# Performance work log

Measured on AMD Instinct MI355X. Metric: run time of the kernel, lower is better.

## Reference

```python
import jax, jax.numpy as jnp
import numpy as np

N_WAY = 5
NKPTS = 17
EMBED = 512
N_SUPPORT = 25  # 5-way 5-shot
N_QUERY = 65536


def setup_inputs() -> dict:
    key = jax.random.key(0)
    ks = jax.random.split(key, 12)
    def lin(k, fan_in, fan_out):
        return jax.random.normal(k, (fan_in, fan_out), jnp.float32) / np.float32(np.sqrt(fan_in))
    return {
        'support_features': jax.random.normal(ks[0], (1, N_SUPPORT, EMBED), jnp.float32),
        'support_keypoints': jax.random.uniform(ks[1], (N_SUPPORT, NKPTS, 2), jnp.float32),
        'query_features': jax.random.normal(ks[2], (N_QUERY, EMBED), jnp.float32),
        'image_coords': jax.random.uniform(ks[3], (N_QUERY, 2), jnp.float32) * 512.0,
        'W1': lin(ks[4], EMBED, EMBED), 'b1': jnp.zeros((EMBED,), jnp.float32),
        'W2': lin(ks[5], EMBED, EMBED), 'b2': jnp.zeros((EMBED,), jnp.float32),
        'Wo1': lin(ks[6], EMBED, EMBED // 2), 'bo1': jnp.zeros((EMBED // 2,), jnp.float32),
        'Wo2': lin(ks[7], EMBED // 2, 2), 'bo2': jnp.zeros((2,), jnp.float32),
        'Wc1': lin(ks[8], EMBED, EMBED // 2), 'bc1': jnp.zeros((EMBED // 2,), jnp.float32),
        'Wc2': lin(ks[9], EMBED // 2, 1), 'bc2': jnp.zeros((1,), jnp.float32),
        'temperature': jnp.float32(1.0),
    }


def reference(support_features, support_keypoints, query_features, image_coords,
              W1, b1, W2, b2, Wo1, bo1, Wo2, bo2, Wc1, bc1, Wc2, bc2, temperature):
    eps = 1e-8
    nkpts = support_keypoints.shape[1]
    n_query = query_features.shape[0]
    D = query_features.shape[-1]

    # --- compute_prototypes (batch_size == 1; per-kpt prototype identical by construction) ---
    sf = support_features.reshape(-1, D)                      # [Ns, D]
    h = jnp.maximum(sf @ W1 + b1, 0.0) @ W2 + b2              # prototype_net MLP
    n_per = h.shape[0] // N_WAY
    proto_way = h.reshape(N_WAY, n_per, D).mean(axis=1)       # [n_way, D]
    prototypes = jnp.broadcast_to(proto_way[:, None, :], (N_WAY, nkpts, D))

    # --- compute_distances: 1 - cosine_sim, scaled by temperature ---
    qn = jnp.linalg.norm(query_features, axis=-1)             # [Nq]
    pn = jnp.linalg.norm(proto_way, axis=-1)                  # [n_way]
    sim = (query_features @ proto_way.T) / jnp.maximum(qn[:, None] * pn[None, :], eps)
    dist_way = (1.0 - sim) / temperature                      # [Nq, n_way]
    distances = jnp.broadcast_to(dist_way[:, :, None], (n_query, N_WAY, nkpts))

    # --- predict_keypoints ---
    # avg over kpts is a no-op (identical per kpt); argmin over ways
    class_predictions = jnp.argmin(dist_way, axis=1)          # [Nq] int
    # softmax over a single scalar == 1.0, so keypoints == offset broadcast over kpts
    offset = jnp.maximum(query_features @ Wo1 + bo1, 0.0) @ Wo2 + bo2   # [Nq, 2]
    conf = jax.nn.sigmoid(jnp.maximum(query_features @ Wc1 + bc1, 0.0) @ Wc2 + bc2)  # [Nq, 1]
    keypoints = jnp.broadcast_to(offset[:, None, :], (n_query, nkpts, 2))
    keypoints = jax.nn.sigmoid(keypoints) * image_coords[:, None, :]    # image_coords provided
    confidence = jnp.broadcast_to(conf, (n_query, nkpts))

    return keypoints, confidence, distances, class_predictions, prototypes
```

## Files before the change

### kernel.cpp

```cpp
#include <hip/hip_runtime.h>
#include <hip/hip_bf16.h>

#define NQ 65536
#define DIM 512
#define HID 256
#define NWAY 5
#define NKPTS 17

typedef short bf16x8 __attribute__((ext_vector_type(8)));
typedef float f32x4 __attribute__((ext_vector_type(4)));
typedef _Float16 half8 __attribute__((ext_vector_type(8)));

static __device__ __forceinline__ unsigned short f2bf(float f) {
    unsigned int x = __float_as_uint(f);
    unsigned int r = (x + 0x7fffu + ((x >> 16) & 1u)) >> 16;
    return (unsigned short)r;
}

static __device__ __forceinline__ void async16(void* l, const void* g) {
    __builtin_amdgcn_global_load_lds(
        (const __attribute__((address_space(1))) unsigned int*)g,
        (__attribute__((address_space(3))) unsigned int*)l, 16, 0, 0);
}

__global__ __launch_bounds__(256) void k_sup(const float* __restrict__ sf,
                                             const float* __restrict__ W1, const float* __restrict__ b1,
                                             float* __restrict__ ws_h1) {
    __shared__ float sfl[512];
    __shared__ float red[4][64];
    int bx = blockIdx.x;
    int s = bx >> 3, cb = bx & 7;
    int t = threadIdx.x;
    if (t < 128) ((float4*)sfl)[t] = ((const float4*)(sf + s * DIM))[t];
    __syncthreads();
    int c = cb * 64 + (t & 63);
    int qd = t >> 6;
    const float* Wp = W1 + (size_t)qd * 128 * DIM + c;
    float acc = 0.0f;
    #pragma unroll 4
    for (int kk = 0; kk < 128; kk++)
        acc += sfl[qd * 128 + kk] * Wp[(size_t)kk * DIM];
    red[qd][t & 63] = acc;
    __syncthreads();
    if (t < 64) {
        float h = red[0][t] + red[1][t] + red[2][t] + red[3][t] + b1[cb * 64 + t];
        ws_h1[s * DIM + cb * 64 + t] = fmaxf(h, 0.0f);
    }
}

__global__ __launch_bounds__(256) void k_mid2(const float* __restrict__ ws_h1,
                                              const float* __restrict__ W2, const float* __restrict__ b2,
                                              const float* __restrict__ Wo1, const float* __restrict__ Wc1,
                                              float* __restrict__ ws_proto, unsigned short* __restrict__ wb) {
    int bx = blockIdx.x;
    int t = threadIdx.x;
    if (bx < 40) {
        __shared__ float ml[512];
        __shared__ float red[4][64];
        int w = bx >> 3, cb = bx & 7;
        for (int i = t; i < 512; i += 256) {
            float sum = 0.0f;
            #pragma unroll
            for (int s5 = 0; s5 < 5; s5++) sum += ws_h1[(w * 5 + s5) * DIM + i];
            ml[i] = sum * 0.2f;
        }
        __syncthreads();
        int c = cb * 64 + (t & 63);
        int qd = t >> 6;
        const float* Wp = W2 + (size_t)qd * 128 * DIM + c;
        float acc = 0.0f;
        #pragma unroll 4
        for (int kk = 0; kk < 128; kk++)
            acc += ml[qd * 128 + kk] * Wp[(size_t)kk * DIM];
        red[qd][t & 63] = acc;
        __syncthreads();
        if (t < 64)
            ws_proto[w * DIM + cb * 64 + t] =
                red[0][t] + red[1][t] + red[2][t] + red[3][t] + b2[cb * 64 + t];
    } else {
        __shared__ unsigned short T[64][72];
        int tb = bx - 40;
        const float* src = (tb < 32) ? Wo1 : Wc1;
        int cofs = (tb < 32) ? 0 : 256;
        int tt = tb & 31;
        int kt = tt >> 2;
        int ct = tt & 3;
        int i = t >> 2;
        int qd = t & 3;
        const float* rp = src + (size_t)(kt * 64 + i) * HID + ct * 64 + qd * 16;
        #pragma unroll
        for (int v = 0; v < 4; v++) {
            float4 x = *(const float4*)(rp + v * 4);
            T[qd * 16 + v * 4 + 0][i] = f2bf(x.x);
            T[qd * 16 + v * 4 + 1][i] = f2bf(x.y);
            T[qd * 16 + v * 4 + 2][i] = f2bf(x.z);
            T[qd * 16 + v * 4 + 3][i] = f2bf(x.w);
        }
        __syncthreads();
        int j = t >> 2;
        int part = t & 3;
        uint4 o0 = *(const uint4*)&T[j][part * 16];
        uint4 o1 = *(const uint4*)&T[j][part * 16 + 8];
        unsigned short* dst = wb + (size_t)(cofs + ct * 64 + j) * DIM + kt * 64 + part * 16;
        *(uint4*)dst = o0;
        *(uint4*)(dst + 8) = o1;
    }
}

__global__ __launch_bounds__(256) void k_prep(const float* __restrict__ qf,
                                              const float* __restrict__ ws_proto,
                                              const float* __restrict__ temp_p,
                                              unsigned short* __restrict__ qbf,
                                              float* __restrict__ out_dist, float* __restrict__ out_class,
                                              float* __restrict__ out_proto) {
    __shared__ float dlds[32 * NWAY];
    int bx = blockIdx.x, t = threadIdx.x;
    int wv = t >> 6, lane = t & 63;

    if (bx < NWAY * NKPTS && t < 128) {
        f32x4 v = *(const f32x4*)(ws_proto + (bx / NKPTS) * DIM + t * 4);
        *(f32x4*)(out_proto + (size_t)bx * DIM + t * 4) = v;
    }

    float p[NWAY][8];
    float pn[NWAY];
    {
        float pp[NWAY];
        #pragma unroll
        for (int w = 0; w < NWAY; w++) {
            f32x4 a = *(const f32x4*)(ws_proto + w * DIM + lane * 8);
            f32x4 b = *(const f32x4*)(ws_proto + w * DIM + lane * 8 + 4);
            p[w][0] = a[0]; p[w][1] = a[1]; p[w][2] = a[2]; p[w][3] = a[3];
            p[w][4] = b[0]; p[w][5] = b[1]; p[w][6] = b[2]; p[w][7] = b[3];
            float s = 0.0f;
            #pragma unroll
            for (int j = 0; j < 8; j++) s += p[w][j] * p[w][j];
            pp[w] = s;
        }
        #pragma unroll
        for (int off = 32; off > 0; off >>= 1) {
            #pragma unroll
            for (int w = 0; w < NWAY; w++) pp[w] += __shfl_xor(pp[w], off, 64);
        }
        #pragma unroll
        for (int w = 0; w < NWAY; w++) pn[w] = sqrtf(pp[w]);
    }
    float invt = 1.0f / temp_p[0];

    int qbase = bx * 32 + wv * 8;
    const float* qp = qf + (size_t)qbase * DIM + lane * 8;
    unsigned short* qb = qbf + (size_t)qbase * DIM + lane * 8;

    float dq[8][NWAY + 1];
    #pragma unroll
    for (int qi = 0; qi < 8; qi++) {
        float4 v0 = *(const float4*)(qp + qi * DIM);
        float4 v1 = *(const float4*)(qp + qi * DIM + 4);
        unsigned int r0 = f2bf(v0.x) | ((unsigned int)f2bf(v0.y) << 16);
        unsigned int r1 = f2bf(v0.z) | ((unsigned int)f2bf(v0.w) << 16);
        unsigned int r2 = f2bf(v1.x) | ((unsigned int)f2bf(v1.y) << 16);
        unsigned int r3 = f2bf(v1.z) | ((unsigned int)f2bf(v1.w) << 16);
        *(uint4*)(qb + qi * DIM) = make_uint4(r0, r1, r2, r3);
        float av[8] = {v0.x, v0.y, v0.z, v0.w, v1.x, v1.y, v1.z, v1.w};
        #pragma unroll
        for (int w = 0; w < NWAY; w++) {
            float s = 0.0f;
            #pragma unroll
            for (int j = 0; j < 8; j++) s += av[j] * p[w][j];
            dq[qi][w] = s;
        }
        float s = 0.0f;
        #pragma unroll
        for (int j = 0; j < 8; j++) s += av[j] * av[j];
        dq[qi][NWAY] = s;
    }
    #pragma unroll
    for (int off = 32; off > 0; off >>= 1) {
        #pragma unroll
        for (int qi = 0; qi < 8; qi++) {
            #pragma unroll
            for (int j = 0; j < NWAY + 1; j++)
                dq[qi][j] += __shfl_xor(dq[qi][j], off, 64);
        }
    }
    if (lane < 8) {
        #pragma unroll
        for (int qi = 0; qi < 8; qi++) {
            if (lane == qi) {
                float qn = sqrtf(dq[qi][NWAY]);
                float mv = 1e30f; int ami = 0;
                #pragma unroll
                for (int w = 0; w < NWAY; w++) {
                    float den = fmaxf(qn * pn[w], 1e-8f);
                    float dd = (1.0f - dq[qi][w] / den) * invt;
                    dlds[(wv * 8 + qi) * NWAY + w] = dd;
                    if (dd < mv) { mv = dd; ami = w; }
                }
                out_class[qbase + qi] = (float)ami;
            }
        }
    }
    __syncthreads();
    int Q0 = bx * 32;
    for (int i = t; i < 32 * NWAY * NKPTS; i += 256) {
        int q2 = i / (NWAY * NKPTS);
        int rem = i - q2 * (NWAY * NKPTS);
        out_dist[(size_t)(Q0 + q2) * (NWAY * NKPTS) + rem] = dlds[q2 * NWAY + rem / NKPTS];
    }
}

__global__ __launch_bounds__(512) void k_gemm(const unsigned short* __restrict__ qbf,
                                              const unsigned short* __restrict__ wb,
                                              const float* __restrict__ bo1, const float* __restrict__ Wo2,
                                              const float* __restrict__ bo2,
                                              const float* __restrict__ bc1, const float* __restrict__ Wc2,
                                              const float* __restrict__ bc2,
                                              const float* __restrict__ ic,
                                              float* __restrict__ out_kp, float* __restrict__ out_conf) {
    __shared__ __align__(16) char smem[81920];
    char* Abase = smem;
    char* Bbase = smem + 16384;

    int mb = blockIdx.x;
    int t = threadIdx.x;
    int wv = t >> 6, lane = t & 63;
    int wr = wv >> 2, wc = wv & 3;
    int r = lane & 15, hq = lane >> 4;

    int srow = lane >> 2;
    int sg = (lane & 3) ^ (srow & 3);
    const unsigned short* Ag = qbf + ((size_t)mb * 128 + wv * 16 + srow) * DIM + sg * 8;
    const unsigned short* Bg = wb + ((size_t)wv * 64 + srow) * DIM + sg * 8;

    f32x4 acc[4][8];
    #pragma unroll
    for (int i2 = 0; i2 < 4; i2++)
        #pragma unroll
        for (int j2 = 0; j2 < 8; j2++) { f32x4 z = {0.0f, 0.0f, 0.0f, 0.0f}; acc[i2][j2] = z; }

    async16(Abase + wv * 1024, Ag);
    #pragma unroll
    for (int i = 0; i < 4; i++)
        async16(Bbase + wv * 4096 + i * 1024, Bg + (size_t)i * 16 * DIM);
    __syncthreads();

    for (int it = 0; it < 16; it++) {
        int par = it & 1;
        if (it < 15) {
            int ko = (it + 1) * 32;
            int np = par ^ 1;
            async16(Abase + np * 8192 + wv * 1024, Ag + ko);
            #pragma unroll
            for (int i = 0; i < 4; i++)
                async16(Bbase + np * 32768 + wv * 4096 + i * 1024, Bg + (size_t)i * 16 * DIM + ko);
        }
        const unsigned short* Ap = (const unsigned short*)(Abase + par * 8192);
        const unsigned short* Bp = (const unsigned short*)(Bbase + par * 32768);
        int sl = (hq ^ (r & 3)) * 8;
        bf16x8 af[4], bfr[8];
        #pragma unroll
        for (int mt = 0; mt < 4; mt++) {
            int m = wr * 64 + mt * 16 + r;
            af[mt] = *(const bf16x8*)(Ap + m * 32 + sl);
        }
        #pragma unroll
        for (int nt = 0; nt < 8; nt++) {
            int c = wc * 128 + nt * 16 + r;
            bfr[nt] = *(const bf16x8*)(Bp + c * 32 + sl);
        }
        #pragma unroll
        for (int mt = 0; mt < 4; mt++)
            #pragma unroll
            for (int nt = 0; nt < 8; nt++)
                acc[mt][nt] = __builtin_amdgcn_mfma_f32_16x16x32_bf16(af[mt], bfr[nt], acc[mt][nt], 0, 0, 0);
        __syncthreads();
    }

    _Float16* hl = (_Float16*)smem;
    float* redf = (float*)(smem + 67584);

    if (wc < 2) {
        #pragma unroll
        for (int nt = 0; nt < 8; nt++) {
            int cl = wc * 128 + nt * 16 + r;
            float bv = bo1[cl];
            #pragma unroll
            for (int mt = 0; mt < 4; mt++)
                #pragma unroll
                for (int rg = 0; rg < 4; rg++) {
                    int ml = wr * 64 + mt * 16 + hq * 4 + rg;
                    hl[ml * 264 + cl] = (_Float16)fmaxf(acc[mt][nt][rg] + bv, 0.0f);
                }
        }
    }
    __syncthreads();
    {
        int q = t & 127, qt = t >> 7;
        float ox = 0.0f, oy = 0.0f;
        #pragma unroll 2
        for (int j0 = 0; j0 < 64; j0 += 8) {
            half8 hv = *(const half8*)(hl + q * 264 + qt * 64 + j0);
            #pragma unroll
            for (int j = 0; j < 8; j++) {
                float2 w2 = *(const float2*)(Wo2 + (qt * 64 + j0 + j) * 2);
                float hf = (float)hv[j];
                ox += hf * w2.x;
                oy += hf * w2.y;
            }
        }
        redf[(qt * 128 + q) * 2] = ox;
        redf[(qt * 128 + q) * 2 + 1] = oy;
    }
    __syncthreads();
    if (t < 128) {
        float sx = bo2[0], sy = bo2[1];
        #pragma unroll
        for (int k2 = 0; k2 < 4; k2++) {
            sx += redf[(k2 * 128 + t) * 2];
            sy += redf[(k2 * 128 + t) * 2 + 1];
        }
        size_t Q = (size_t)mb * 128 + t;
        float2 icv = *(const float2*)(ic + Q * 2);
        float gx = icv.x / (1.0f + __expf(-sx));
        float gy = icv.y / (1.0f + __expf(-sy));
        float2 g2 = make_float2(gx, gy);
        float2* dst = (float2*)(out_kp + Q * 34);
        #pragma unroll
        for (int k2 = 0; k2 < 17; k2++) dst[k2] = g2;
    }
    if (wc >= 2) {
        #pragma unroll
        for (int nt = 0; nt < 8; nt++) {
            int cl = (wc - 2) * 128 + nt * 16 + r;
            float bv = bc1[cl];
            #pragma unroll
            for (int mt = 0; mt < 4; mt++)
                #pragma unroll
                for (int rg = 0; rg < 4; rg++) {
                    int ml = wr * 64 + mt * 16 + hq * 4 + rg;
                    hl[ml * 264 + cl] = (_Float16)fmaxf(acc[mt][nt][rg] + bv, 0.0f);
                }
        }
    }
    __syncthreads();
    {
        int q = t & 127, qt = t >> 7;
        float cs = 0.0f;
        #pragma unroll 2
        for (int j0 = 0; j0 < 64; j0 += 8) {
            half8 hv = *(const half8*)(hl + q * 264 + qt * 64 + j0);
            #pragma unroll
            for (int j = 0; j < 8; j++)
                cs += (float)hv[j] * Wc2[qt * 64 + j0 + j];
        }
        redf[qt * 128 + q] = cs;
    }
    __syncthreads();
    if (t < 128) {
        float s = bc2[0] + redf[t] + redf[128 + t] + redf[256 + t] + redf[384 + t];
        float sg2 = 1.0f / (1.0f + __expf(-s));
        size_t Q = (size_t)mb * 128 + t;
        float* dst = out_conf + Q * 17;
        #pragma unroll
        for (int k2 = 0; k2 < 17; k2++) dst[k2] = sg2;
    }
}

extern "C" void kernel_launch(void* const* d_in, const int* in_sizes, int n_in,
                              void* d_out, int out_size, void* d_ws, size_t ws_size,
                              hipStream_t stream) {
    const float* sf = (const float*)d_in[0];
    const float* qf = (const float*)d_in[2];
    const float* ic = (const float*)d_in[3];
    const float* W1 = (const float*)d_in[4];
    const float* b1 = (const float*)d_in[5];
    const float* W2 = (const float*)d_in[6];
    const float* b2 = (const float*)d_in[7];
    const float* Wo1 = (const float*)d_in[8];
    const float* bo1 = (const float*)d_in[9];
    const float* Wo2 = (const float*)d_in[10];
    const float* bo2 = (const float*)d_in[11];
    const float* Wc1 = (const float*)d_in[12];
    const float* bc1 = (const float*)d_in[13];
    const float* Wc2 = (const float*)d_in[14];
    const float* bc2 = (const float*)d_in[15];
    const float* temp = (const float*)d_in[16];

    float* out = (float*)d_out;
    float* out_kp = out;
    float* out_conf = out + 2228224;
    float* out_dist = out + 3342336;
    float* out_class = out + 8912896;
    float* out_proto = out + 8978432;

    char* ws = (char*)d_ws;
    float* ws_h1 = (float*)ws;
    float* ws_proto = (float*)(ws + 51200);
    unsigned short* ws_wb = (unsigned short*)(ws + 65536);
    unsigned short* ws_qbf = (unsigned short*)(ws + 1048576);

    hipLaunchKernelGGL(k_sup, dim3(200), dim3(256), 0, stream, sf, W1, b1, ws_h1);
    hipLaunchKernelGGL(k_mid2, dim3(104), dim3(256), 0, stream, ws_h1, W2, b2, Wo1, Wc1, ws_proto, ws_wb);
    hipLaunchKernelGGL(k_prep, dim3(2048), dim3(256), 0, stream, qf, ws_proto, temp,
                       ws_qbf, out_dist, out_class, out_proto);
    hipLaunchKernelGGL(k_gemm, dim3(512), dim3(512), 0, stream, ws_qbf, ws_wb,
                       bo1, Wo2, bo2, bc1, Wc2, bc2, ic, out_kp, out_conf);
}
```

Before: 341.0 us.

## Fuse query prep (bf16 convert, cosine distances) into the GEMM kernel

Merges the k_prep kernel into the GEMM kernel. Each block now loads fp32 query rows directly, converts them to bf16 into LDS, and accumulates prototype dot products and norms alongside the MFMA loop. This removes the bf16 query round-trip through workspace (a 64 MB write plus read) and one kernel launch. In exchange, the A-tile staging becomes synchronous register loads instead of async LDS loads, LDS use grows (which may limit occupancy), and the distance output writes now sit in the GEMM epilogue.

```diff
diff --git a/kernel.cpp b/kernel.cpp
--- a/kernel.cpp
+++ b/kernel.cpp
@@ -107,119 +107,26 @@
     }
 }
 
-__global__ __launch_bounds__(256) void k_prep(const float* __restrict__ qf,
-                                              const float* __restrict__ ws_proto,
-                                              const float* __restrict__ temp_p,
-                                              unsigned short* __restrict__ qbf,
-                                              float* __restrict__ out_dist, float* __restrict__ out_class,
-                                              float* __restrict__ out_proto) {
-    __shared__ float dlds[32 * NWAY];
-    int bx = blockIdx.x, t = threadIdx.x;
-    int wv = t >> 6, lane = t & 63;
-
-    if (bx < NWAY * NKPTS && t < 128) {
-        f32x4 v = *(const f32x4*)(ws_proto + (bx / NKPTS) * DIM + t * 4);
-        *(f32x4*)(out_proto + (size_t)bx * DIM + t * 4) = v;
-    }
-
-    float p[NWAY][8];
-    float pn[NWAY];
-    {
-        float pp[NWAY];
-        #pragma unroll
-        for (int w = 0; w < NWAY; w++) {
-            f32x4 a = *(const f32x4*)(ws_proto + w * DIM + lane * 8);
-            f32x4 b = *(const f32x4*)(ws_proto + w * DIM + lane * 8 + 4);
-            p[w][0] = a[0]; p[w][1] = a[1]; p[w][2] = a[2]; p[w][3] = a[3];
-            p[w][4] = b[0]; p[w][5] = b[1]; p[w][6] = b[2]; p[w][7] = b[3];
-            float s = 0.0f;
-            #pragma unroll
-            for (int j = 0; j < 8; j++) s += p[w][j] * p[w][j];
-            pp[w] = s;
-        }
-        #pragma unroll
-        for (int off = 32; off > 0; off >>= 1) {
-            #pragma unroll
-            for (int w = 0; w < NWAY; w++) pp[w] += __shfl_xor(pp[w], off, 64);
-        }
-        #pragma unroll
-        for (int w = 0; w < NWAY; w++) pn[w] = sqrtf(pp[w]);
-    }
-    float invt = 1.0f / temp_p[0];
-
-    int qbase = bx * 32 + wv * 8;
-    const float* qp = qf + (size_t)qbase * DIM + lane * 8;
-    unsigned short* qb = qbf + (size_t)qbase * DIM + lane * 8;
-
-    float dq[8][NWAY + 1];
-    #pragma unroll
-    for (int qi = 0; qi < 8; qi++) {
-        float4 v0 = *(const float4*)(qp + qi * DIM);
-        float4 v1 = *(const float4*)(qp + qi * DIM + 4);
-        unsigned int r0 = f2bf(v0.x) | ((unsigned int)f2bf(v0.y) << 16);
-        unsigned int r1 = f2bf(v0.z) | ((unsigned int)f2bf(v0.w) << 16);
-        unsigned int r2 = f2bf(v1.x) | ((unsigned int)f2bf(v1.y) << 16);
-        unsigned int r3 = f2bf(v1.z) | ((unsigned int)f2bf(v1.w) << 16);
-        *(uint4*)(qb + qi * DIM) = make_uint4(r0, r1, r2, r3);
-        float av[8] = {v0.x, v0.y, v0.z, v0.w, v1.x, v1.y, v1.z, v1.w};
-        #pragma unroll
-        for (int w = 0; w < NWAY; w++) {
-            float s = 0.0f;
-            #pragma unroll
-            for (int j = 0; j < 8; j++) s += av[j] * p[w][j];
-            dq[qi][w] = s;
-        }
-        float s = 0.0f;
-        #pragma unroll
-        for (int j = 0; j < 8; j++) s += av[j] * av[j];
-        dq[qi][NWAY] = s;
-    }
-    #pragma unroll
-    for (int off = 32; off > 0; off >>= 1) {
-        #pragma unroll
-        for (int qi = 0; qi < 8; qi++) {
-            #pragma unroll
-            for (int j = 0; j < NWAY + 1; j++)
-                dq[qi][j] += __shfl_xor(dq[qi][j], off, 64);
-        }
-    }
-    if (lane < 8) {
-        #pragma unroll
-        for (int qi = 0; qi < 8; qi++) {
-            if (lane == qi) {
-                float qn = sqrtf(dq[qi][NWAY]);
-                float mv = 1e30f; int ami = 0;
-                #pragma unroll
-                for (int w = 0; w < NWAY; w++) {
-                    float den = fmaxf(qn * pn[w], 1e-8f);
-                    float dd = (1.0f - dq[qi][w] / den) * invt;
-                    dlds[(wv * 8 + qi) * NWAY + w] = dd;
-                    if (dd < mv) { mv = dd; ami = w; }
-                }
-                out_class[qbase + qi] = (float)ami;
-            }
-        }
-    }
-    __syncthreads();
-    int Q0 = bx * 32;
-    for (int i = t; i < 32 * NWAY * NKPTS; i += 256) {
-        int q2 = i / (NWAY * NKPTS);
-        int rem = i - q2 * (NWAY * NKPTS);
-        out_dist[(size_t)(Q0 + q2) * (NWAY * NKPTS) + rem] = dlds[q2 * NWAY + rem / NKPTS];
-    }
-}
-
-__global__ __launch_bounds__(512) void k_gemm(const unsigned short* __restrict__ qbf,
-                                              const unsigned short* __restrict__ wb,
-                                              const float* __restrict__ bo1, const float* __restrict__ Wo2,
-                                              const float* __restrict__ bo2,
-                                              const float* __restrict__ bc1, const float* __restrict__ Wc2,
-                                              const float* __restrict__ bc2,
-                                              const float* __restrict__ ic,
-                                              float* __restrict__ out_kp, float* __restrict__ out_conf) {
-    __shared__ __align__(16) char smem[81920];
+__global__ __launch_bounds__(512, 2) void k_fused2(const float* __restrict__ qf,
+                                                   const unsigned short* __restrict__ wb,
+                                                   const float* __restrict__ ws_proto,
+                                                   const float* __restrict__ temp_p,
+                                                   const float* __restrict__ bo1, const float* __restrict__ Wo2,
+                                                   const float* __restrict__ bo2,
+                                                   const float* __restrict__ bc1, const float* __restrict__ Wc2,
+                                                   const float* __restrict__ bc2,
+                                                   const float* __restrict__ ic,
+                                                   float* __restrict__ out_kp, float* __restrict__ out_conf,
+                                                   float* __restrict__ out_dist, float* __restrict__ out_class,
+                                                   float* __restrict__ out_proto) {
+    __shared__ __align__(16) char smem[94752];
     char* Abase = smem;
     char* Bbase = smem + 16384;
+    float* s_proto = (float*)(smem + 81920);
+    float* pn_lds = (float*)(smem + 92160);
+    float* dlds = (float*)(smem + 92192);
+    _Float16* hl = (_Float16*)smem;
+    float* redf = (float*)(smem + 67584);
 
     int mb = blockIdx.x;
     int t = threadIdx.x;
@@ -227,58 +134,92 @@
     int wr = wv >> 2, wc = wv & 3;
     int r = lane & 15, hq = lane >> 4;
 
+    for (int i = t; i < NWAY * DIM; i += 512) s_proto[i] = ws_proto[i];
+    if (mb < NWAY * NKPTS && t < 128) {
+        f32x4 v = *(const f32x4*)(ws_proto + (mb / NKPTS) * DIM + t * 4);
+        *(f32x4*)(out_proto + (size_t)mb * DIM + t * 4) = v;
+    }
+    float invt = 1.0f / temp_p[0];
+
     int srow = lane >> 2;
     int sg = (lane & 3) ^ (srow & 3);
-    const unsigned short* Ag = qbf + ((size_t)mb * 128 + wv * 16 + srow) * DIM + sg * 8;
     const unsigned short* Bg = wb + ((size_t)wv * 64 + srow) * DIM + sg * 8;
+
+    int am = t >> 2, akc = t & 3;
+    const float* Ag = qf + ((size_t)mb * 128 + am) * DIM + akc * 8;
+    int awoff = am * 64 + ((akc ^ (am & 3)) * 16);
 
     f32x4 acc[4][8];
     #pragma unroll
     for (int i2 = 0; i2 < 4; i2++)
         #pragma unroll
         for (int j2 = 0; j2 < 8; j2++) { f32x4 z = {0.0f, 0.0f, 0.0f, 0.0f}; acc[i2][j2] = z; }
-
-    async16(Abase + wv * 1024, Ag);
+    float ds[NWAY] = {0, 0, 0, 0, 0};
+    float qq = 0.0f;
+
+    float4 a0 = *(const float4*)(Ag);
+    float4 a1 = *(const float4*)(Ag + 4);
     #pragma unroll
     for (int i = 0; i < 4; i++)
         async16(Bbase + wv * 4096 + i * 1024, Bg + (size_t)i * 16 * DIM);
-    __syncthreads();
-
+
+    #pragma unroll 2
     for (int it = 0; it < 16; it++) {
         int par = it & 1;
+        unsigned int p0 = f2bf(a0.x) | ((unsigned int)f2bf(a0.y) << 16);
+        unsigned int p1 = f2bf(a0.z) | ((unsigned int)f2bf(a0.w) << 16);
+        unsigned int p2 = f2bf(a1.x) | ((unsigned int)f2bf(a1.y) << 16);
+        unsigned int p3 = f2bf(a1.z) | ((unsigned int)f2bf(a1.w) << 16);
+        *(uint4*)(Abase + par * 8192 + awoff) = make_uint4(p0, p1, p2, p3);
+        float av[8] = {a0.x, a0.y, a0.z, a0.w, a1.x, a1.y, a1.z, a1.w};
+        int kb = it * 32 + akc * 8;
+        #pragma unroll
+        for (int w = 0; w < NWAY; w++) {
+            f32x4 pv0 = *(const f32x4*)(s_proto + w * DIM + kb);
+            f32x4 pv1 = *(const f32x4*)(s_proto + w * DIM + kb + 4);
+            ds[w] += av[0] * pv0[0] + av[1] * pv0[1] + av[2] * pv0[2] + av[3] * pv0[3]
+                   + av[4] * pv1[0] + av[5] * pv1[1] + av[6] * pv1[2] + av[7] * pv1[3];
+        }
+        #pragma unroll
+        for (int j = 0; j < 8; j++) qq += av[j] * av[j];
         if (it < 15) {
             int ko = (it + 1) * 32;
-            int np = par ^ 1;
-            async16(Abase + np * 8192 + wv * 1024, Ag + ko);
+            a0 = *(const float4*)(Ag + ko);
+            a1 = *(const float4*)(Ag + ko + 4);
             #pragma unroll
             for (int i = 0; i < 4; i++)
-                async16(Bbase + np * 32768 + wv * 4096 + i * 1024, Bg + (size_t)i * 16 * DIM + ko);
-        }
+                async16(Bbase + (par ^ 1) * 32768 + wv * 4096 + i * 1024,
+                        Bg + (size_t)i * 16 * DIM + ko);
+        }
+        __syncthreads();
         const unsigned short* Ap = (const unsigned short*)(Abase + par * 8192);
         const unsigned short* Bp = (const unsigned short*)(Bbase + par * 32768);
         int sl = (hq ^ (r & 3)) * 8;
         bf16x8 af[4], bfr[8];
         #pragma unroll
-        for (int mt = 0; mt < 4; mt++) {
-            int m = wr * 64 + mt * 16 + r;
-            af[mt] = *(const bf16x8*)(Ap + m * 32 + sl);
-        }
-        #pragma unroll
-        for (int nt = 0; nt < 8; nt++) {
-            int c = wc * 128 + nt * 16 + r;
-            bfr[nt] = *(const bf16x8*)(Bp + c * 32 + sl);
-        }
+        for (int mt = 0; mt < 4; mt++)
+            af[mt] = *(const bf16x8*)(Ap + (wr * 64 + mt * 16 + r) * 32 + sl);
+        #pragma unroll
+        for (int nt = 0; nt < 8; nt++)
+            bfr[nt] = *(const bf16x8*)(Bp + (wc * 128 + nt * 16 + r) * 32 + sl);
         #pragma unroll
         for (int mt = 0; mt < 4; mt++)
             #pragma unroll
             for (int nt = 0; nt < 8; nt++)
                 acc[mt][nt] = __builtin_amdgcn_mfma_f32_16x16x32_bf16(af[mt], bfr[nt], acc[mt][nt], 0, 0, 0);
-        __syncthreads();
-    }
-
-    _Float16* hl = (_Float16*)smem;
-    float* redf = (float*)(smem + 67584);
-
+    }
+
+    __syncthreads();
+
+    if (wv < NWAY) {
+        f32x4 a = *(const f32x4*)(s_proto + wv * DIM + lane * 8);
+        f32x4 b = *(const f32x4*)(s_proto + wv * DIM + lane * 8 + 4);
+        float ss = a[0]*a[0] + a[1]*a[1] + a[2]*a[2] + a[3]*a[3]
+                 + b[0]*b[0] + b[1]*b[1] + b[2]*b[2] + b[3]*b[3];
+        #pragma unroll
+        for (int off = 32; off > 0; off >>= 1) ss += __shfl_xor(ss, off, 64);
+        if (lane == 0) pn_lds[wv] = sqrtf(ss);
+    }
     if (wc < 2) {
         #pragma unroll
         for (int nt = 0; nt < 8; nt++) {
@@ -294,6 +235,25 @@
         }
     }
     __syncthreads();
+
+    #pragma unroll
+    for (int off = 1; off <= 2; off <<= 1) {
+        #pragma unroll
+        for (int w = 0; w < NWAY; w++) ds[w] += __shfl_xor(ds[w], off, 64);
+        qq += __shfl_xor(qq, off, 64);
+    }
+    if (akc == 0) {
+        float qn = sqrtf(qq);
+        float mv = 1e30f; int ami = 0;
+        #pragma unroll
+        for (int w = 0; w < NWAY; w++) {
+            float den = fmaxf(qn * pn_lds[w], 1e-8f);
+            float d = (1.0f - ds[w] / den) * invt;
+            dlds[am * 5 + w] = d;
+            if (d < mv) { mv = d; ami = w; }
+        }
+        out_class[mb * 128 + am] = (float)ami;
+    }
     {
         int q = t & 127, qt = t >> 7;
         float ox = 0.0f, oy = 0.0f;
@@ -312,6 +272,7 @@
         redf[(qt * 128 + q) * 2 + 1] = oy;
     }
     __syncthreads();
+
     if (t < 128) {
         float sx = bo2[0], sy = bo2[1];
         #pragma unroll
@@ -342,7 +303,13 @@
                 }
         }
     }
-    __syncthreads();
+    for (int i = t; i < 128 * NWAY * NKPTS; i += 512) {
+        int q2 = i / (NWAY * NKPTS);
+        int rem = i - q2 * (NWAY * NKPTS);
+        out_dist[(size_t)(mb * 128 + q2) * (NWAY * NKPTS) + rem] = dlds[q2 * 5 + rem / NKPTS];
+    }
+    __syncthreads();
+
     {
         int q = t & 127, qt = t >> 7;
         float cs = 0.0f;
@@ -397,12 +364,10 @@
     float* ws_h1 = (float*)ws;
     float* ws_proto = (float*)(ws + 51200);
     unsigned short* ws_wb = (unsigned short*)(ws + 65536);
-    unsigned short* ws_qbf = (unsigned short*)(ws + 1048576);
 
     hipLaunchKernelGGL(k_sup, dim3(200), dim3(256), 0, stream, sf, W1, b1, ws_h1);
     hipLaunchKernelGGL(k_mid2, dim3(104), dim3(256), 0, stream, ws_h1, W2, b2, Wo1, Wc1, ws_proto, ws_wb);
-    hipLaunchKernelGGL(k_prep, dim3(2048), dim3(256), 0, stream, qf, ws_proto, temp,
-                       ws_qbf, out_dist, out_class, out_proto);
-    hipLaunchKernelGGL(k_gemm, dim3(512), dim3(512), 0, stream, ws_qbf, ws_wb,
-                       bo1, Wo2, bo2, bc1, Wc2, bc2, ic, out_kp, out_conf);
-}
+    hipLaunchKernelGGL(k_fused2, dim3(512), dim3(512), 0, stream, qf, ws_wb, ws_proto, temp,
+                       bo1, Wo2, bo2, bc1, Wc2, bc2, ic, out_kp, out_conf,
+                       out_dist, out_class, out_proto);
+}
```

Result: faster. 319.1 us (-6.4%).
